# Optimization experiments

Measured on AMD Instinct MI355X. Metric: run time of the kernel, lower is better.

## Reference

```python
import jax, jax.numpy as jnp
import numpy as np

N = 100000
F_IN = 128
H = 128
E = 1600000
EP = 200000


def _gcn_conv(x, W, b, src, dst, n):
    # GCNConv (PyG default): add self-loops done by caller; symmetric norm; linear + scatter-add.
    xw = x @ W                                        # [n, H]
    deg = jax.ops.segment_sum(jnp.ones(src.shape[0], x.dtype), dst, num_segments=n)
    dinv = jnp.where(deg > 0, jax.lax.rsqrt(deg), 0.0)
    norm = dinv[src] * dinv[dst]                      # [E']
    msg = xw[src] * norm[:, None]                     # [E', H] gather
    out = jax.ops.segment_sum(msg, dst, num_segments=n)  # scatter-add
    return out + b


def setup_inputs() -> dict:
    key = jax.random.key(0)
    k = jax.random.split(key, 9)
    x = jax.random.normal(k[0], (N, F_IN), dtype=jnp.float32)
    edge_index = jax.random.randint(k[1], (2, E), 0, N, dtype=jnp.int64)
    dict_node = jax.random.randint(k[2], (N,), 0, N, dtype=jnp.int64)
    pos_edge_index = jax.random.randint(k[3], (2, EP), 0, N, dtype=jnp.int64)
    neg_edge_index = jax.random.randint(k[4], (2, EP), 0, N, dtype=jnp.int64)
    s1 = 1.0 / np.sqrt(F_IN)
    s2 = 1.0 / np.sqrt(H)
    W1 = jax.random.uniform(k[5], (F_IN, H), jnp.float32, -s1, s1)
    b1 = jnp.zeros((H,), jnp.float32)
    W2 = jax.random.uniform(k[6], (H, H), jnp.float32, -s2, s2)
    b2 = jnp.zeros((H,), jnp.float32)
    return {"x": x, "W1": W1, "b1": b1, "W2": W2, "b2": b2,
            "edge_index": edge_index, "dict_node": dict_node,
            "pos_edge_index": pos_edge_index, "neg_edge_index": neg_edge_index}


def reference(x, W1, b1, W2, b2, edge_index, dict_node, pos_edge_index, neg_edge_index):
    n = x.shape[0]
    # add self-loops once (both convs use the same edge_index)
    loop = jnp.arange(n, dtype=edge_index.dtype)
    src = jnp.concatenate([edge_index[0], loop])
    dst = jnp.concatenate([edge_index[1], loop])
    # encode (dropout p=0.01 is identity in eval mode)
    h = jax.nn.relu(_gcn_conv(x, W1, b1, src, dst, n))
    h = jax.nn.relu(_gcn_conv(h, W2, b2, src, dst, n))
    # global_mean_pool over dict_node segments (size = num_nodes)
    sums = jax.ops.segment_sum(h, dict_node, num_segments=n)
    cnt = jax.ops.segment_sum(jnp.ones((n,), h.dtype), dict_node, num_segments=n)
    z = sums / jnp.maximum(cnt, 1.0)[:, None]
    # decode: per-edge dot products over concatenated pos/neg edges
    ei = jnp.concatenate([pos_edge_index, neg_edge_index], axis=-1)
    logits = jnp.sum(z[ei[0]] * z[ei[1]], axis=-1)
    return logits
```

## Files before the change

### kernel.cpp

```cpp
#include <hip/hip_runtime.h>
#include <hip/hip_fp16.h>

#define HH 128
#define PCHUNK 16384


__global__ __launch_bounds__(256) void part_count_k(const int* __restrict__ key, int e,
                                                    int nbkt, int nblk,
                                                    int* __restrict__ gcnt,
                                                    int* __restrict__ blkoff) {
  __shared__ int h[512];
  for (int i = threadIdx.x; i < nbkt; i += 256) h[i] = 0;
  __syncthreads();
  int start = blockIdx.x * PCHUNK;
  int cnt = e - start; if (cnt > PCHUNK) cnt = PCHUNK;
  for (int i = threadIdx.x; i < cnt; i += 256)
    atomicAdd(&h[key[start + i] >> 8], 1);
  __syncthreads();
  for (int i = threadIdx.x; i < nbkt; i += 256) {
    int c = h[i];
    if (c) blkoff[(size_t)i * nblk + blockIdx.x] = atomicAdd(&gcnt[i], c);
  }
}

__global__ __launch_bounds__(512) void scan_bkt_k(const int* __restrict__ gcnt,
                                                  int* __restrict__ bktbase, int nbkt, int e) {
  __shared__ int sc[512];
  int tid = threadIdx.x;
  int v = (tid < nbkt) ? gcnt[tid] : 0;
  sc[tid] = v;
  __syncthreads();
  for (int off = 1; off < 512; off <<= 1) {
    int t = (tid >= off) ? sc[tid - off] : 0;
    __syncthreads();
    sc[tid] += t;
    __syncthreads();
  }
  if (tid < nbkt) bktbase[tid] = sc[tid] - v;
  if (tid == 0) bktbase[nbkt] = e;
}

__global__ __launch_bounds__(256) void part_scatter_k(const int* __restrict__ src,
                                                      const int* __restrict__ key, int e,
                                                      int nbkt, int nblk,
                                                      const int* __restrict__ bktbase,
                                                      const int* __restrict__ blkoff,
                                                      int* __restrict__ part) {
  __shared__ int cur[512];
  for (int i = threadIdx.x; i < nbkt; i += 256)
    cur[i] = bktbase[i] + blkoff[(size_t)i * nblk + blockIdx.x];
  __syncthreads();
  int start = blockIdx.x * PCHUNK;
  int cnt = e - start; if (cnt > PCHUNK) cnt = PCHUNK;
  for (int i = threadIdx.x; i < cnt; i += 256) {
    int d = key[start + i], s = src[start + i];
    int pos = atomicAdd(&cur[d >> 8], 1);
    part[pos] = (s << 8) | (d & 255);
  }
}

__global__ __launch_bounds__(256) void part_scatter_idx_k(const int* __restrict__ key, int e,
                                                          int nbkt, int nblk,
                                                          const int* __restrict__ bktbase,
                                                          const int* __restrict__ blkoff,
                                                          int* __restrict__ part) {
  __shared__ int cur[512];
  for (int i = threadIdx.x; i < nbkt; i += 256)
    cur[i] = bktbase[i] + blkoff[(size_t)i * nblk + blockIdx.x];
  __syncthreads();
  int start = blockIdx.x * PCHUNK;
  int cnt = e - start; if (cnt > PCHUNK) cnt = PCHUNK;
  for (int i = threadIdx.x; i < cnt; i += 256) {
    int d = key[start + i];
    int pos = atomicAdd(&cur[d >> 8], 1);
    part[pos] = ((start + i) << 8) | (d & 255);
  }
}

__global__ __launch_bounds__(256) void bucket_csr_k(const int* __restrict__ part,
                                                    const int* __restrict__ bktbase,
                                                    int* __restrict__ rowptr,
                                                    float* __restrict__ dinv,
                                                    int* __restrict__ esrc,
                                                    int n, int e, int nbkt) {
  __shared__ int hist[256];
  __shared__ int sc[256];
  __shared__ int cur[256];
  int tid = threadIdx.x;
  int b = blockIdx.x;
  int dstbase = b << 8;
  int nloc = n - dstbase; if (nloc > 256) nloc = 256;
  int beg = bktbase[b], bend = bktbase[b + 1];

  hist[tid] = 0;
  __syncthreads();
  for (int j = beg + tid; j < bend; j += 256)
    atomicAdd(&hist[part[j] & 255], 1);
  __syncthreads();
  int v = hist[tid];
  sc[tid] = v;
  __syncthreads();
  for (int off = 1; off < 256; off <<= 1) {
    int t = (tid >= off) ? sc[tid - off] : 0;
    __syncthreads();
    sc[tid] += t;
    __syncthreads();
  }
  int excl = sc[tid] - v;
  if (tid < nloc) {
    rowptr[dstbase + tid] = beg + excl;
    cur[tid] = beg + excl;
    if (dinv) dinv[dstbase + tid] = rsqrtf((float)v + 1.0f);
  }
  __syncthreads();
  for (int j = beg + tid; j < bend; j += 256) {
    int p = part[j];
    int pos = atomicAdd(&cur[p & 255], 1);
    esrc[pos] = p >> 8;
  }
  if (b == nbkt - 1 && tid == 0) rowptr[n] = e;
}

template <bool OUT16>
__global__ __launch_bounds__(256) void gemm128_v4(const float* __restrict__ A,
                                                  const float* __restrict__ W,
                                                  const float* __restrict__ dscale,
                                                  void* __restrict__ out, int n) {
  __shared__ float As[64][65];
  const int tid = threadIdx.x;
  const int rbase = blockIdx.x * 64;
  const int vrows = (n - rbase) < 64 ? (n - rbase) : 64;

  const int r = tid & 63;
  const int q = __builtin_amdgcn_readfirstlane(tid >> 6);
  const float* Wq = W + q * 32;

  float4 acc[8];
  #pragma unroll
  for (int c = 0; c < 8; ++c) acc[c] = make_float4(0.f, 0.f, 0.f, 0.f);

  #pragma unroll
  for (int ph = 0; ph < 2; ++ph) {
    if (ph) __syncthreads();
    #pragma unroll
    for (int j = 0; j < 4; ++j) {
      int f = tid + 256 * j;
      int rr = f >> 4, c4 = f & 15;
      float4 v = (rr < vrows)
          ? ((const float4*)(A + (size_t)(rbase + rr) * HH + ph * 64))[c4]
          : make_float4(0.f, 0.f, 0.f, 0.f);
      As[rr][c4 * 4 + 0] = v.x;
      As[rr][c4 * 4 + 1] = v.y;
      As[rr][c4 * 4 + 2] = v.z;
      As[rr][c4 * 4 + 3] = v.w;
    }
    __syncthreads();

    #pragma unroll 4
    for (int kk = 0; kk < 64; ++kk) {
      float a = As[r][kk];
      const float4* Wr = (const float4*)(Wq + (size_t)(ph * 64 + kk) * HH);
      #pragma unroll
      for (int c = 0; c < 8; ++c) {
        float4 w = Wr[c];
        acc[c].x += a * w.x; acc[c].y += a * w.y;
        acc[c].z += a * w.z; acc[c].w += a * w.w;
      }
    }
  }

  int row = rbase + r;
  if (row < n) {
    float s = dscale ? dscale[row] : 1.0f;
    if (OUT16) {
      uint2* o = (uint2*)((__half*)out + (size_t)row * HH) + q * 8;
      #pragma unroll
      for (int c = 0; c < 8; ++c) {
        __half2 h0 = __float22half2_rn(make_float2(acc[c].x * s, acc[c].y * s));
        __half2 h1 = __float22half2_rn(make_float2(acc[c].z * s, acc[c].w * s));
        uint2 u;
        u.x = *reinterpret_cast<unsigned*>(&h0);
        u.y = *reinterpret_cast<unsigned*>(&h1);
        o[c] = u;
      }
    } else {
      float4* o = (float4*)((float*)out + (size_t)row * HH + q * 32);
      #pragma unroll
      for (int c = 0; c < 8; ++c) {
        acc[c].x *= s; acc[c].y *= s; acc[c].z *= s; acc[c].w *= s;
        o[c] = acc[c];
      }
    }
  }
}

template <bool HOUT16>
__global__ __launch_bounds__(256) void gather16_k(const __half* __restrict__ xw16,
                                                  const int* __restrict__ rowptr,
                                                  const int* __restrict__ esrc,
                                                  const float* __restrict__ dinv,
                                                  const float* __restrict__ bias,
                                                  void* __restrict__ h, int n) {
  int wid = (int)((blockIdx.x * (size_t)blockDim.x + threadIdx.x) >> 6);
  int lane = threadIdx.x & 63;
  if (wid >= n) return;
  int beg = rowptr[wid], end = rowptr[wid + 1];
  int half = lane >> 5, l32 = lane & 31;
  const uint2* base = (const uint2*)xw16 + l32;
  float4 acc = make_float4(0.f, 0.f, 0.f, 0.f);

  for (int j0 = beg; j0 < end; j0 += 64) {
    int myj = j0 + lane;
    int sv = (myj < end) ? esrc[myj] : 0;
    int cnt = end - j0; if (cnt > 64) cnt = 64;
    int k = 0;
    for (; k + 8 <= cnt; k += 8) {
      #pragma unroll
      for (int p = 0; p < 4; ++p) {
        int sa = __builtin_amdgcn_readlane(sv, k + 2 * p);
        int sb = __builtin_amdgcn_readlane(sv, k + 2 * p + 1);
        unsigned off = (unsigned)(half ? sb : sa) << 5;
        uint2 u = base[off];
        float2 f0 = __half22float2(*reinterpret_cast<__half2*>(&u.x));
        float2 f1 = __half22float2(*reinterpret_cast<__half2*>(&u.y));
        acc.x += f0.x; acc.y += f0.y; acc.z += f1.x; acc.w += f1.y;
      }
    }
    for (; k + 2 <= cnt; k += 2) {
      int sa = __builtin_amdgcn_readlane(sv, k);
      int sb = __builtin_amdgcn_readlane(sv, k + 1);
      unsigned off = (unsigned)(half ? sb : sa) << 5;
      uint2 u = base[off];
      float2 f0 = __half22float2(*reinterpret_cast<__half2*>(&u.x));
      float2 f1 = __half22float2(*reinterpret_cast<__half2*>(&u.y));
      acc.x += f0.x; acc.y += f0.y; acc.z += f1.x; acc.w += f1.y;
    }
    if (k < cnt) {
      int sa = __builtin_amdgcn_readlane(sv, k);
      if (half == 0) {
        uint2 u = base[(unsigned)sa << 5];
        float2 f0 = __half22float2(*reinterpret_cast<__half2*>(&u.x));
        float2 f1 = __half22float2(*reinterpret_cast<__half2*>(&u.y));
        acc.x += f0.x; acc.y += f0.y; acc.z += f1.x; acc.w += f1.y;
      }
    }
  }
  acc.x += __shfl_xor(acc.x, 32);
  acc.y += __shfl_xor(acc.y, 32);
  acc.z += __shfl_xor(acc.z, 32);
  acc.w += __shfl_xor(acc.w, 32);
  if (half == 0) {
    uint2 u = base[(unsigned)wid << 5];
    float2 s0 = __half22float2(*reinterpret_cast<__half2*>(&u.x));
    float2 s1 = __half22float2(*reinterpret_cast<__half2*>(&u.y));
    float di = dinv[wid];
    float4 bb = ((const float4*)bias)[l32];
    float4 o;
    o.x = fmaxf(bb.x + di * (acc.x + s0.x), 0.f);
    o.y = fmaxf(bb.y + di * (acc.y + s0.y), 0.f);
    o.z = fmaxf(bb.z + di * (acc.z + s1.x), 0.f);
    o.w = fmaxf(bb.w + di * (acc.w + s1.y), 0.f);
    if (HOUT16) {
      __half2 p0 = __float22half2_rn(make_float2(o.x, o.y));
      __half2 p1 = __float22half2_rn(make_float2(o.z, o.w));
      uint2 w;
      w.x = *reinterpret_cast<unsigned*>(&p0);
      w.y = *reinterpret_cast<unsigned*>(&p1);
      ((uint2*)h)[((size_t)wid << 5) + l32] = w;
    } else {
      ((float4*)h)[((size_t)wid << 5) + l32] = o;
    }
  }
}

__global__ __launch_bounds__(256) void decode_fused4_k(const __half* __restrict__ h2,
                                                       const int* __restrict__ rowptr,
                                                       const int* __restrict__ nodelist,
                                                       const int* __restrict__ pos,
                                                       const int* __restrict__ neg,
                                                       float* __restrict__ out, int ep) {
  int wv = (int)((blockIdx.x * (size_t)blockDim.x + threadIdx.x) >> 6);
  int lane = threadIdx.x & 63;
  int qq = lane >> 4, l16 = lane & 15;
  int e0 = wv * 2;
  if (e0 >= 2 * ep) return;
  int edge = e0 + (qq >> 1);
  int side = qq & 1;
  bool live = edge < 2 * ep;
  int eL = live ? edge : 2 * ep - 1;
  int node;
  if (eL < ep) node = side ? pos[ep + eL] : pos[eL];
  else { int t = eL - ep; node = side ? neg[ep + t] : neg[t]; }

  int beg = rowptr[node], end = rowptr[node + 1];
  const uint2* h4 = (const uint2*)h2;
  float4 a0 = make_float4(0.f, 0.f, 0.f, 0.f);
  float4 a1 = make_float4(0.f, 0.f, 0.f, 0.f);
  float4 c0 = make_float4(0.f, 0.f, 0.f, 0.f);
  float4 c1 = make_float4(0.f, 0.f, 0.f, 0.f);

  for (int j = beg; j < end; j += 2) {
    bool two = (j + 1) < end;
    int m0 = nodelist[j];
    int m1 = two ? nodelist[j + 1] : m0;
    const uint2* r0 = h4 + ((size_t)m0 << 5);
    const uint2* r1 = h4 + ((size_t)m1 << 5);
    uint2 u0 = r0[l16], u1 = r0[l16 + 16];
    uint2 v0 = r1[l16], v1 = r1[l16 + 16];
    float2 f;
    f = __half22float2(*reinterpret_cast<__half2*>(&u0.x)); a0.x += f.x; a0.y += f.y;
    f = __half22float2(*reinterpret_cast<__half2*>(&u0.y)); a0.z += f.x; a0.w += f.y;
    f = __half22float2(*reinterpret_cast<__half2*>(&u1.x)); a1.x += f.x; a1.y += f.y;
    f = __half22float2(*reinterpret_cast<__half2*>(&u1.y)); a1.z += f.x; a1.w += f.y;
    if (two) {
      f = __half22float2(*reinterpret_cast<__half2*>(&v0.x)); c0.x += f.x; c0.y += f.y;
      f = __half22float2(*reinterpret_cast<__half2*>(&v0.y)); c0.z += f.x; c0.w += f.y;
      f = __half22float2(*reinterpret_cast<__half2*>(&v1.x)); c1.x += f.x; c1.y += f.y;
      f = __half22float2(*reinterpret_cast<__half2*>(&v1.y)); c1.z += f.x; c1.w += f.y;
    }
  }
  a0.x += c0.x; a0.y += c0.y; a0.z += c0.z; a0.w += c0.w;
  a1.x += c1.x; a1.y += c1.y; a1.z += c1.z; a1.w += c1.w;

  float inv = 1.0f / fmaxf((float)(end - beg), 1.0f);
  a0.x *= inv; a0.y *= inv; a0.z *= inv; a0.w *= inv;
  a1.x *= inv; a1.y *= inv; a1.z *= inv; a1.w *= inv;

  float4 b0, b1;
  b0.x = __shfl_xor(a0.x, 16); b0.y = __shfl_xor(a0.y, 16);
  b0.z = __shfl_xor(a0.z, 16); b0.w = __shfl_xor(a0.w, 16);
  b1.x = __shfl_xor(a1.x, 16); b1.y = __shfl_xor(a1.y, 16);
  b1.z = __shfl_xor(a1.z, 16); b1.w = __shfl_xor(a1.w, 16);
  float p = a0.x * b0.x + a0.y * b0.y + a0.z * b0.z + a0.w * b0.w
          + a1.x * b1.x + a1.y * b1.y + a1.z * b1.z + a1.w * b1.w;
  #pragma unroll
  for (int off = 8; off > 0; off >>= 1) p += __shfl_xor(p, off);
  if (live && side == 0 && l16 == 0) out[edge] = p;
}

__global__ void fill_deg_k(float* __restrict__ deg, int n) {
  int i = blockIdx.x * blockDim.x + threadIdx.x;
  if (i < n) deg[i] = 1.0f;
}
__global__ void accum_deg_k(const int* __restrict__ dst, float* __restrict__ deg, int e) {
  int i = blockIdx.x * blockDim.x + threadIdx.x;
  if (i < e) atomicAdd(&deg[dst[i]], 1.0f);
}
__global__ void dinv_k(float* __restrict__ deg, int n) {
  int i = blockIdx.x * blockDim.x + threadIdx.x;
  if (i < n) deg[i] = rsqrtf(deg[i]);
}
__global__ void init_h_k(const float* __restrict__ xw, const float* __restrict__ bias,
                         const float* __restrict__ dinv, float* __restrict__ h, int n) {
  int gid = blockIdx.x * blockDim.x + threadIdx.x;
  int node = gid >> 5, c4 = gid & 31;
  if (node >= n) return;
  float di = dinv[node];
  float nm = di * di;
  float4 v = ((const float4*)(xw + (size_t)node * HH))[c4];
  float4 b = ((const float4*)bias)[c4];
  ((float4*)(h + (size_t)node * HH))[c4] =
      make_float4(b.x + nm * v.x, b.y + nm * v.y, b.z + nm * v.z, b.w + nm * v.w);
}
__global__ void scatter_k(const float* __restrict__ xw, float* __restrict__ h,
                          const float* __restrict__ dinv, const int* __restrict__ src,
                          const int* __restrict__ dst, int e) {
  int gid = blockIdx.x * blockDim.x + threadIdx.x;
  int edge = gid >> 5, lane = gid & 31;
  if (edge >= e) return;
  int s = src[edge], d = dst[edge];
  float norm = dinv[s] * dinv[d];
  float4 v = ((const float4*)(xw + (size_t)s * HH))[lane];
  float* o = h + (size_t)d * HH + lane * 4;
  atomicAdd(o + 0, norm * v.x);
  atomicAdd(o + 1, norm * v.y);
  atomicAdd(o + 2, norm * v.z);
  atomicAdd(o + 3, norm * v.w);
}
__global__ void relu_k(float4* __restrict__ h, int n4) {
  int i = blockIdx.x * blockDim.x + threadIdx.x;
  if (i < n4) {
    float4 v = h[i];
    v.x = fmaxf(v.x, 0.f); v.y = fmaxf(v.y, 0.f);
    v.z = fmaxf(v.z, 0.f); v.w = fmaxf(v.w, 0.f);
    h[i] = v;
  }
}
__global__ void pool_accum_k(const float* __restrict__ h, const int* __restrict__ dict,
                             float* __restrict__ z, float* __restrict__ cnt, int n) {
  int gid = blockIdx.x * blockDim.x + threadIdx.x;
  int node = gid >> 5, lane = gid & 31;
  if (node >= n) return;
  int d = dict[node];
  float4 v = ((const float4*)(h + (size_t)node * HH))[lane];
  float* o = z + (size_t)d * HH + lane * 4;
  atomicAdd(o + 0, v.x); atomicAdd(o + 1, v.y);
  atomicAdd(o + 2, v.z); atomicAdd(o + 3, v.w);
  if (lane == 0) atomicAdd(&cnt[d], 1.0f);
}
__global__ void pool_div_k(float* __restrict__ z, const float* __restrict__ cnt, int n) {
  int gid = blockIdx.x * blockDim.x + threadIdx.x;
  int node = gid >> 5, lane = gid & 31;
  if (node >= n) return;
  float inv = 1.0f / fmaxf(cnt[node], 1.0f);
  float4* p = (float4*)(z + (size_t)node * HH) + lane;
  float4 v = *p;
  v.x *= inv; v.y *= inv; v.z *= inv; v.w *= inv;
  *p = v;
}
__global__ void decode_k(const float* __restrict__ z, const int* __restrict__ pos,
                         const int* __restrict__ neg, float* __restrict__ out, int ep) {
  int gid = blockIdx.x * blockDim.x + threadIdx.x;
  int edge = gid >> 5, lane = gid & 31;
  if (edge >= 2 * ep) return;
  int a, b;
  if (edge < ep) { a = pos[edge];      b = pos[ep + edge]; }
  else           { a = neg[edge - ep]; b = neg[edge]; }
  const float4* za = (const float4*)(z + (size_t)a * HH);
  const float4* zb = (const float4*)(z + (size_t)b * HH);
  float4 va = za[lane], vb = zb[lane];
  float dot = va.x * vb.x + va.y * vb.y + va.z * vb.z + va.w * vb.w;
  #pragma unroll
  for (int off = 16; off > 0; off >>= 1) dot += __shfl_xor(dot, off);
  if (lane == 0) out[edge] = dot;
}

extern "C" void kernel_launch(void* const* d_in, const int* in_sizes, int n_in,
                              void* d_out, int out_size, void* d_ws, size_t ws_size,
                              hipStream_t stream) {
  const float* x  = (const float*)d_in[0];
  const float* W1 = (const float*)d_in[1];
  const float* b1 = (const float*)d_in[2];
  const float* W2 = (const float*)d_in[3];
  const float* b2 = (const float*)d_in[4];
  const int* ei   = (const int*)d_in[5];
  const int* dict = (const int*)d_in[6];
  const int* pe   = (const int*)d_in[7];
  const int* ne   = (const int*)d_in[8];

  const int n  = in_sizes[0] / HH;
  const int e  = in_sizes[5] / 2;
  const int ep = in_sizes[7] / 2;
  const int* src = ei;
  const int* dst = ei + e;

  const size_t nf = (size_t)n * HH;
  const int nbkt  = (n + 255) >> 8;
  const int nblkE = (e + PCHUNK - 1) / PCHUNK;
  const int nblkN = (n + PCHUNK - 1) / PCHUNK;

  float*  p0     = (float*)d_ws;
  float*  bufF   = p0;
  __half* xw16   = (__half*)(p0 + nf);
  float*  dinv   = p0 + nf + nf / 2;
  int*    rowptr = (int*)(dinv + n);
  int*    tmp    = rowptr + (n + 1);
  int*    esrc   = tmp + n;
  int*    bsum   = esrc + e;
  int*    gcnt   = bsum + 256;
  int*    bktbase = gcnt + nbkt;
  size_t need = (nf + nf / 2 + n) * sizeof(float) +
                (size_t)(3 * n + 1 + e + 256 + 2 * nbkt + 1) * sizeof(int);

  int* partE   = (int*)bufF;
  int* blkoffE = (int*)xw16;
  int* partN   = (int*)xw16;
  int* blkoffN = partN + n;

  const int nb    = (n + 255) / 256;
  const int nb32  = (int)(((size_t)n * 32 + 255) / 256);
  const int nb64  = (int)(((size_t)n * 64 + 255) / 256);
  const int gemb  = (n + 63) / 64;
  const int deb2  = (int)(((size_t)ep * 64 + 255) / 256);

  bool fast = (ws_size >= need) && (nbkt <= 512) && (n < (1 << 23)) &&
              ((size_t)e <= nf) && ((size_t)nbkt * nblkE * 2 <= nf);

  if (fast) {
    hipMemsetAsync(gcnt, 0, (size_t)nbkt * sizeof(int), stream);
    part_count_k<<<nblkE, 256, 0, stream>>>(dst, e, nbkt, nblkE, gcnt, blkoffE);
    scan_bkt_k<<<1, 512, 0, stream>>>(gcnt, bktbase, nbkt, e);
    part_scatter_k<<<nblkE, 256, 0, stream>>>(src, dst, e, nbkt, nblkE, bktbase, blkoffE, partE);
    bucket_csr_k<<<nbkt, 256, 0, stream>>>(partE, bktbase, rowptr, dinv, esrc, n, e, nbkt);

    gemm128_v4<true><<<gemb, 256, 0, stream>>>(x, W1, dinv, xw16, n);
    gather16_k<false><<<nb64, 256, 0, stream>>>(xw16, rowptr, esrc, dinv, b1, bufF, n);
    gemm128_v4<true><<<gemb, 256, 0, stream>>>(bufF, W2, dinv, xw16, n);
    __half* h2_16 = (__half*)bufF;
    gather16_k<true><<<nb64, 256, 0, stream>>>(xw16, rowptr, esrc, dinv, b2, h2_16, n);

    hipMemsetAsync(gcnt, 0, (size_t)nbkt * sizeof(int), stream);
    part_count_k<<<nblkN, 256, 0, stream>>>(dict, n, nbkt, nblkN, gcnt, blkoffN);
    scan_bkt_k<<<1, 512, 0, stream>>>(gcnt, bktbase, nbkt, n);
    part_scatter_idx_k<<<nblkN, 256, 0, stream>>>(dict, n, nbkt, nblkN, bktbase, blkoffN, partN);
    bucket_csr_k<<<nbkt, 256, 0, stream>>>(partN, bktbase, rowptr, nullptr, esrc, n, n, nbkt);

    decode_fused4_k<<<deb2, 256, 0, stream>>>(h2_16, rowptr, esrc, pe, ne, (float*)d_out, ep);
  } else {
    float* bufA  = (float*)d_ws;
    float* bufB  = bufA + nf;
    float* dinv2 = bufB + nf;
    float* cnt   = dinv2 + n;
    fill_deg_k<<<nb, 256, 0, stream>>>(dinv2, n);
    accum_deg_k<<<(e + 255) / 256, 256, 0, stream>>>(dst, dinv2, e);
    dinv_k<<<nb, 256, 0, stream>>>(dinv2, n);

    gemm128_v4<false><<<gemb, 256, 0, stream>>>(x, W1, nullptr, bufA, n);
    init_h_k<<<nb32, 256, 0, stream>>>(bufA, b1, dinv2, bufB, n);
    scatter_k<<<(int)(((size_t)e * 32 + 255) / 256), 256, 0, stream>>>(bufA, bufB, dinv2, src, dst, e);
    relu_k<<<nb32, 256, 0, stream>>>((float4*)bufB, n * 32);

    gemm128_v4<false><<<gemb, 256, 0, stream>>>(bufB, W2, nullptr, bufA, n);
    init_h_k<<<nb32, 256, 0, stream>>>(bufA, b2, dinv2, bufB, n);
    scatter_k<<<(int)(((size_t)e * 32 + 255) / 256), 256, 0, stream>>>(bufA, bufB, dinv2, src, dst, e);
    relu_k<<<nb32, 256, 0, stream>>>((float4*)bufB, n * 32);

    hipMemsetAsync(bufA, 0, nf * sizeof(float), stream);
    hipMemsetAsync(cnt, 0, (size_t)n * sizeof(float), stream);
    pool_accum_k<<<nb32, 256, 0, stream>>>(bufB, dict, bufA, cnt, n);
    pool_div_k<<<nb32, 256, 0, stream>>>(bufA, cnt, n);
    decode_k<<<(int)(((size_t)2 * ep * 32 + 255) / 256), 256, 0, stream>>>(
        bufA, pe, ne, (float*)d_out, ep);
  }
}
```

Measured before the change: 398.1 us.

## Split fused pool+decode into separate mean-pool and edge dot-product kernels

Replaces the fused decode kernel, which recomputed each endpoint's mean-pooled vector from its dict_node segment for every edge, with a pooling kernel that writes z in fp16 once per node, followed by a simple decode kernel that gathers two z rows per edge. This stops redundant segment gathers when a node appears in many edges, at the cost of an extra kernel launch and a z write/read round trip. The partition scratch is moved to another part of bufF so that z can live in xw16, and the fast-path condition gets a matching size check. z is now rounded to fp16 before the dot product, which adds a small precision loss.

```diff
diff --git a/kernel.cpp b/kernel.cpp
--- a/kernel.cpp
+++ b/kernel.cpp
@@ -273,69 +273,53 @@
   }
 }
 
-__global__ __launch_bounds__(256) void decode_fused4_k(const __half* __restrict__ h2,
-                                                       const int* __restrict__ rowptr,
-                                                       const int* __restrict__ nodelist,
-                                                       const int* __restrict__ pos,
-                                                       const int* __restrict__ neg,
-                                                       float* __restrict__ out, int ep) {
-  int wv = (int)((blockIdx.x * (size_t)blockDim.x + threadIdx.x) >> 6);
-  int lane = threadIdx.x & 63;
-  int qq = lane >> 4, l16 = lane & 15;
-  int e0 = wv * 2;
-  if (e0 >= 2 * ep) return;
-  int edge = e0 + (qq >> 1);
-  int side = qq & 1;
-  bool live = edge < 2 * ep;
-  int eL = live ? edge : 2 * ep - 1;
-  int node;
-  if (eL < ep) node = side ? pos[ep + eL] : pos[eL];
-  else { int t = eL - ep; node = side ? neg[ep + t] : neg[t]; }
-
-  int beg = rowptr[node], end = rowptr[node + 1];
+__global__ __launch_bounds__(256) void pool16_k(const __half* __restrict__ h2,
+                                                const int* __restrict__ rowptr,
+                                                const int* __restrict__ nodelist,
+                                                __half* __restrict__ z, int n) {
+  int gid = blockIdx.x * blockDim.x + threadIdx.x;
+  int g = gid >> 5, l32 = gid & 31;
+  if (g >= n) return;
+  int beg = rowptr[g], end = rowptr[g + 1];
   const uint2* h4 = (const uint2*)h2;
-  float4 a0 = make_float4(0.f, 0.f, 0.f, 0.f);
-  float4 a1 = make_float4(0.f, 0.f, 0.f, 0.f);
-  float4 c0 = make_float4(0.f, 0.f, 0.f, 0.f);
-  float4 c1 = make_float4(0.f, 0.f, 0.f, 0.f);
-
-  for (int j = beg; j < end; j += 2) {
-    bool two = (j + 1) < end;
-    int m0 = nodelist[j];
-    int m1 = two ? nodelist[j + 1] : m0;
-    const uint2* r0 = h4 + ((size_t)m0 << 5);
-    const uint2* r1 = h4 + ((size_t)m1 << 5);
-    uint2 u0 = r0[l16], u1 = r0[l16 + 16];
-    uint2 v0 = r1[l16], v1 = r1[l16 + 16];
-    float2 f;
-    f = __half22float2(*reinterpret_cast<__half2*>(&u0.x)); a0.x += f.x; a0.y += f.y;
-    f = __half22float2(*reinterpret_cast<__half2*>(&u0.y)); a0.z += f.x; a0.w += f.y;
-    f = __half22float2(*reinterpret_cast<__half2*>(&u1.x)); a1.x += f.x; a1.y += f.y;
-    f = __half22float2(*reinterpret_cast<__half2*>(&u1.y)); a1.z += f.x; a1.w += f.y;
-    if (two) {
-      f = __half22float2(*reinterpret_cast<__half2*>(&v0.x)); c0.x += f.x; c0.y += f.y;
-      f = __half22float2(*reinterpret_cast<__half2*>(&v0.y)); c0.z += f.x; c0.w += f.y;
-      f = __half22float2(*reinterpret_cast<__half2*>(&v1.x)); c1.x += f.x; c1.y += f.y;
-      f = __half22float2(*reinterpret_cast<__half2*>(&v1.y)); c1.z += f.x; c1.w += f.y;
-    }
-  }
-  a0.x += c0.x; a0.y += c0.y; a0.z += c0.z; a0.w += c0.w;
-  a1.x += c1.x; a1.y += c1.y; a1.z += c1.z; a1.w += c1.w;
-
+  float4 a = make_float4(0.f, 0.f, 0.f, 0.f);
+  for (int j = beg; j < end; ++j) {
+    int m = nodelist[j];
+    uint2 u = h4[((size_t)m << 5) + l32];
+    float2 f0 = __half22float2(*reinterpret_cast<__half2*>(&u.x));
+    float2 f1 = __half22float2(*reinterpret_cast<__half2*>(&u.y));
+    a.x += f0.x; a.y += f0.y; a.z += f1.x; a.w += f1.y;
+  }
   float inv = 1.0f / fmaxf((float)(end - beg), 1.0f);
-  a0.x *= inv; a0.y *= inv; a0.z *= inv; a0.w *= inv;
-  a1.x *= inv; a1.y *= inv; a1.z *= inv; a1.w *= inv;
-
-  float4 b0, b1;
-  b0.x = __shfl_xor(a0.x, 16); b0.y = __shfl_xor(a0.y, 16);
-  b0.z = __shfl_xor(a0.z, 16); b0.w = __shfl_xor(a0.w, 16);
-  b1.x = __shfl_xor(a1.x, 16); b1.y = __shfl_xor(a1.y, 16);
-  b1.z = __shfl_xor(a1.z, 16); b1.w = __shfl_xor(a1.w, 16);
-  float p = a0.x * b0.x + a0.y * b0.y + a0.z * b0.z + a0.w * b0.w
-          + a1.x * b1.x + a1.y * b1.y + a1.z * b1.z + a1.w * b1.w;
+  __half2 p0 = __float22half2_rn(make_float2(a.x * inv, a.y * inv));
+  __half2 p1 = __float22half2_rn(make_float2(a.z * inv, a.w * inv));
+  uint2 w;
+  w.x = *reinterpret_cast<unsigned*>(&p0);
+  w.y = *reinterpret_cast<unsigned*>(&p1);
+  ((uint2*)z)[((size_t)g << 5) + l32] = w;
+}
+
+__global__ __launch_bounds__(256) void decode16_k(const __half* __restrict__ z,
+                                                  const int* __restrict__ pos,
+                                                  const int* __restrict__ neg,
+                                                  float* __restrict__ out, int ep) {
+  int gid = blockIdx.x * blockDim.x + threadIdx.x;
+  int edge = gid >> 5, l32 = gid & 31;
+  if (edge >= 2 * ep) return;
+  int a, b;
+  if (edge < ep) { a = pos[edge];      b = pos[ep + edge]; }
+  else           { int t = edge - ep; a = neg[t]; b = neg[ep + t]; }
+  const uint2* z4 = (const uint2*)z;
+  uint2 ua = z4[((size_t)a << 5) + l32];
+  uint2 ub = z4[((size_t)b << 5) + l32];
+  float2 fa0 = __half22float2(*reinterpret_cast<__half2*>(&ua.x));
+  float2 fa1 = __half22float2(*reinterpret_cast<__half2*>(&ua.y));
+  float2 fb0 = __half22float2(*reinterpret_cast<__half2*>(&ub.x));
+  float2 fb1 = __half22float2(*reinterpret_cast<__half2*>(&ub.y));
+  float dot = fa0.x * fb0.x + fa0.y * fb0.y + fa1.x * fb1.x + fa1.y * fb1.y;
   #pragma unroll
-  for (int off = 8; off > 0; off >>= 1) p += __shfl_xor(p, off);
-  if (live && side == 0 && l16 == 0) out[edge] = p;
+  for (int off = 16; off > 0; off >>= 1) dot += __shfl_xor(dot, off);
+  if (l32 == 0) out[edge] = dot;
 }
 
 __global__ void fill_deg_k(float* __restrict__ deg, int n) {
@@ -464,17 +448,18 @@
 
   int* partE   = (int*)bufF;
   int* blkoffE = (int*)xw16;
-  int* partN   = (int*)xw16;
+  int* partN   = (int*)(bufF + nf / 2);
   int* blkoffN = partN + n;
 
   const int nb    = (n + 255) / 256;
   const int nb32  = (int)(((size_t)n * 32 + 255) / 256);
   const int nb64  = (int)(((size_t)n * 64 + 255) / 256);
   const int gemb  = (n + 63) / 64;
-  const int deb2  = (int)(((size_t)ep * 64 + 255) / 256);
+  const int deb   = (int)(((size_t)2 * ep * 32 + 255) / 256);
 
   bool fast = (ws_size >= need) && (nbkt <= 512) && (n < (1 << 23)) &&
-              ((size_t)e <= nf) && ((size_t)nbkt * nblkE * 2 <= nf);
+              ((size_t)e <= nf) && ((size_t)nbkt * nblkE * 2 <= nf) &&
+              ((size_t)(n + nbkt * nblkN) * 2 <= nf);
 
   if (fast) {
     hipMemsetAsync(gcnt, 0, (size_t)nbkt * sizeof(int), stream);
@@ -495,7 +480,9 @@
     part_scatter_idx_k<<<nblkN, 256, 0, stream>>>(dict, n, nbkt, nblkN, bktbase, blkoffN, partN);
     bucket_csr_k<<<nbkt, 256, 0, stream>>>(partN, bktbase, rowptr, nullptr, esrc, n, n, nbkt);
 
-    decode_fused4_k<<<deb2, 256, 0, stream>>>(h2_16, rowptr, esrc, pe, ne, (float*)d_out, ep);
+    __half* z16 = xw16;
+    pool16_k<<<nb32, 256, 0, stream>>>(h2_16, rowptr, esrc, z16, n);
+    decode16_k<<<deb, 256, 0, stream>>>(z16, pe, ne, (float*)d_out, ep);
   } else {
     float* bufA  = (float*)d_ws;
     float* bufB  = bufA + nf;
```

New measurement: 380.9 us. -4.3%, faster.
